# Kernel optimization log

Measured on AMD Instinct MI355X. Metric: run time of the kernel, lower is better.

Reference implementation:

```python
import jax, jax.numpy as jnp
import numpy as np

E = 512; H = 512; L = 3; NH = 8; HD = H // NH; V = 32000
B = 64; S = 64; T = 20


def setup_inputs() -> dict:
    key = jax.random.key(0)
    ks = jax.random.split(key, 14)
    sc = 0.02
    return {
        "encoder_out": jax.random.normal(ks[0], (B, S, H), jnp.float32),
        "captions": jax.random.randint(ks[1], (B, T), 0, V),
        "embed_table": jax.random.normal(ks[2], (V, E), jnp.float32) * sc,
        "w_ih": jax.random.normal(ks[3], (L, 3 * H, E), jnp.float32) * sc,
        "w_hh": jax.random.normal(ks[4], (L, 3 * H, H), jnp.float32) * sc,
        "b_ih": jax.random.normal(ks[5], (L, 3 * H), jnp.float32) * sc,
        "b_hh": jax.random.normal(ks[6], (L, 3 * H), jnp.float32) * sc,
        "in_proj_w": jax.random.normal(ks[7], (3 * H, H), jnp.float32) * sc,
        "in_proj_b": jax.random.normal(ks[8], (3 * H,), jnp.float32) * sc,
        "out_proj_w": jax.random.normal(ks[9], (H, H), jnp.float32) * sc,
        "out_proj_b": jax.random.normal(ks[10], (H,), jnp.float32) * sc,
        "fc_w": jax.random.normal(ks[11], (V, H), jnp.float32) * sc,
        "fc_b": jax.random.normal(ks[12], (V,), jnp.float32) * sc,
    }


def _gru_cell(x, h, Wih, Whh, bih, bhh):
    # PyTorch GRUCell math. x: (B, in), h: (B, H)
    gi = x @ Wih.T + bih  # (B, 3H)
    gh = h @ Whh.T + bhh
    i_r, i_z, i_n = jnp.split(gi, 3, axis=-1)
    h_r, h_z, h_n = jnp.split(gh, 3, axis=-1)
    r = jax.nn.sigmoid(i_r + h_r)
    z = jax.nn.sigmoid(i_z + h_z)
    n = jnp.tanh(i_n + r * h_n)
    return (1.0 - z) * n + z * h


def reference(encoder_out, captions, embed_table, w_ih, w_hh, b_ih, b_hh,
              in_proj_w, in_proj_b, out_proj_w, out_proj_b, fc_w, fc_b):
    Wq, Wk, Wv = jnp.split(in_proj_w, 3, axis=0)
    bq, bk, bv = jnp.split(in_proj_b, 3, axis=0)
    # K/V projections of encoder_out are timestep-invariant: precompute once.
    Kh = (encoder_out @ Wk.T + bk).reshape(B, S, NH, HD)
    Vh = (encoder_out @ Wv.T + bv).reshape(B, S, NH, HD)
    scale = 1.0 / jnp.sqrt(jnp.float32(HD))

    emb = embed_table[captions]              # (B, T, E)
    xs = jnp.transpose(emb, (1, 0, 2))       # (T, B, E)

    def step(h, x_t):
        # h: (L, B, H); x_t: (B, E)
        new_h = []
        inp = x_t
        for l in range(L):
            hl = _gru_cell(inp, h[l], w_ih[l], w_hh[l], b_ih[l], b_hh[l])
            new_h.append(hl)
            inp = hl
        q = (inp @ Wq.T + bq).reshape(B, NH, HD)
        scores = jnp.einsum('bnd,bsnd->bns', q, Kh) * scale
        attn = jax.nn.softmax(scores, axis=-1)
        ctx = jnp.einsum('bns,bsnd->bnd', attn, Vh).reshape(B, H)
        ao = ctx @ out_proj_w.T + out_proj_b
        logits = ao @ fc_w.T + fc_b           # (B, V)
        return jnp.stack(new_h), logits

    h0 = jnp.zeros((L, B, H), dtype=encoder_out.dtype)
    _, logits = jax.lax.scan(step, h0, xs)    # logits: (T, B, V)
    return jnp.transpose(logits, (1, 0, 2))   # (B, T, V)
```

## Files before the change

kernel.cpp:

```cpp
#include <hip/hip_runtime.h>
#include <hip/hip_bf16.h>

#define TT 20
#define BB 64
#define SS 64
#define HH 512
#define EE 512
#define VV 32000

typedef __bf16 bf16x8 __attribute__((ext_vector_type(8)));
typedef float f32x4 __attribute__((ext_vector_type(4)));


__global__ __launch_bounds__(256) void f2bf_kernel(const float* __restrict__ in,
                                                   __hip_bfloat16* __restrict__ out, int n) {
    int i = blockIdx.x * 256 + threadIdx.x;
    if (i < n) out[i] = __float2bfloat16(in[i]);
}

__global__ __launch_bounds__(256) void zero_h_kernel(float* __restrict__ hf,
                                                     __hip_bfloat16* __restrict__ hb, int n) {
    int i = blockIdx.x * 256 + threadIdx.x;
    if (i < n) { hf[i] = 0.f; hb[i] = __float2bfloat16(0.f); }
}

__global__ __launch_bounds__(256) void gather_emb_kernel(const float* __restrict__ tab,
                                                         const int* __restrict__ cap,
                                                         __hip_bfloat16* __restrict__ out) {
    int i = blockIdx.x * 256 + threadIdx.x;
    int e = i & (EE - 1);
    int tb = i >> 9;
    int t = tb >> 6;
    int b = tb & 63;
    int tok = cap[b * TT + t];
    out[i] = __float2bfloat16(tab[(size_t)tok * EE + e]);
}


__global__ __launch_bounds__(256) void gemm_bt_kernel(
    const __hip_bfloat16* __restrict__ A,
    const __hip_bfloat16* __restrict__ Bm,
    const float* __restrict__ bias,
    float* __restrict__ Cf,
    __hip_bfloat16* __restrict__ Cb,
    int K, int ldc, int row_stride, int row_off,
    long sAz, long sBz, long sCz)
{
    A  += (size_t)blockIdx.z * sAz;
    Bm += (size_t)blockIdx.z * sBz;
    long cbase = (long)blockIdx.z * sCz;

    int m0 = blockIdx.x * 64, n0 = blockIdx.y * 64;
    int wave = threadIdx.x >> 6, lane = threadIdx.x & 63;
    int wm = wave & 1, wn = wave >> 1;
    int row16 = lane & 15, quad = lane >> 4;

    const __hip_bfloat16* a0p = A  + (size_t)(m0 + wm * 32 + row16) * K + quad * 8;
    const __hip_bfloat16* a1p = a0p + (size_t)16 * K;
    const __hip_bfloat16* b0p = Bm + (size_t)(n0 + wn * 32 + row16) * K + quad * 8;
    const __hip_bfloat16* b1p = b0p + (size_t)16 * K;

    f32x4 acc00 = {0.f, 0.f, 0.f, 0.f};
    f32x4 acc01 = {0.f, 0.f, 0.f, 0.f};
    f32x4 acc10 = {0.f, 0.f, 0.f, 0.f};
    f32x4 acc11 = {0.f, 0.f, 0.f, 0.f};

    for (int k = 0; k < K; k += 32) {
        bf16x8 a0 = *reinterpret_cast<const bf16x8*>(a0p + k);
        bf16x8 a1 = *reinterpret_cast<const bf16x8*>(a1p + k);
        bf16x8 b0 = *reinterpret_cast<const bf16x8*>(b0p + k);
        bf16x8 b1 = *reinterpret_cast<const bf16x8*>(b1p + k);
        acc00 = __builtin_amdgcn_mfma_f32_16x16x32_bf16(a0, b0, acc00, 0, 0, 0);
        acc01 = __builtin_amdgcn_mfma_f32_16x16x32_bf16(a0, b1, acc01, 0, 0, 0);
        acc10 = __builtin_amdgcn_mfma_f32_16x16x32_bf16(a1, b0, acc10, 0, 0, 0);
        acc11 = __builtin_amdgcn_mfma_f32_16x16x32_bf16(a1, b1, acc11, 0, 0, 0);
    }

    f32x4 accs[2][2] = {{acc00, acc01}, {acc10, acc11}};
#pragma unroll
    for (int mt = 0; mt < 2; ++mt) {
#pragma unroll
        for (int nt = 0; nt < 2; ++nt) {
            int col = n0 + wn * 32 + nt * 16 + row16;
            float bv = bias ? bias[col] : 0.f;
#pragma unroll
            for (int r = 0; r < 4; ++r) {
                int row = m0 + wm * 32 + mt * 16 + quad * 4 + r;
                long off = cbase + (long)(row * row_stride + row_off) * ldc + col;
                float v = accs[mt][nt][r] + bv;
                if (Cb) Cb[off] = __float2bfloat16(v);
                else    Cf[off] = v;
            }
        }
    }
}


__device__ inline float sigmf(float x) { return 1.f / (1.f + __expf(-x)); }

__global__ __launch_bounds__(256) void gru_combine_kernel(
    const float* __restrict__ GI, const float* __restrict__ GH,
    const float* __restrict__ bih, const float* __restrict__ bhh,
    float* __restrict__ h, __hip_bfloat16* __restrict__ hb)
{
    int i = blockIdx.x * 256 + threadIdx.x;
    int b = i >> 9, j = i & 511;
    const float* gi = GI + (size_t)b * 1536;
    const float* gh = GH + (size_t)b * 1536;
    float ir = gi[j]        + bih[j];
    float iz = gi[j + 512]  + bih[j + 512];
    float in_ = gi[j + 1024] + bih[j + 1024];
    float hr = gh[j]        + bhh[j];
    float hz = gh[j + 512]  + bhh[j + 512];
    float hn = gh[j + 1024] + bhh[j + 1024];
    float r = sigmf(ir + hr);
    float z = sigmf(iz + hz);
    float n = tanhf(in_ + r * hn);
    float hv = h[i];
    float hnew = (1.f - z) * n + z * hv;
    h[i] = hnew;
    hb[i] = __float2bfloat16(hnew);
}

__global__ __launch_bounds__(64) void attn_kernel(
    const float* __restrict__ q, const float* __restrict__ KV,
    __hip_bfloat16* __restrict__ ctxb)
{
    int b = blockIdx.x >> 3, nh = blockIdx.x & 7;
    int lane = threadIdx.x;

    const float* qrow = q + (size_t)b * HH + nh * 64;
    const float* kr   = KV + (size_t)(b * 64 + lane) * 1024 + nh * 64;
    float sc = 0.f;
#pragma unroll
    for (int d = 0; d < 64; ++d) sc += qrow[d] * kr[d];
    sc *= 0.125f;

    float m = sc;
    for (int off = 32; off; off >>= 1) m = fmaxf(m, __shfl_xor(m, off, 64));
    float e = __expf(sc - m);
    float s = e;
    for (int off = 32; off; off >>= 1) s += __shfl_xor(s, off, 64);
    float p = e / s;

    __shared__ float pl[64];
    pl[lane] = p;
    __syncthreads();

    float acc = 0.f;
    const float* vb = KV + (size_t)(b * 64) * 1024 + 512 + nh * 64 + lane;
#pragma unroll
    for (int si = 0; si < 64; ++si) acc += pl[si] * vb[(size_t)si * 1024];

    ctxb[(size_t)b * HH + nh * 64 + lane] = __float2bfloat16(acc);
}


extern "C" void kernel_launch(void* const* d_in, const int* in_sizes, int n_in,
                              void* d_out, int out_size, void* d_ws, size_t ws_size,
                              hipStream_t stream) {
    const float* enc        = (const float*)d_in[0];
    const int*   cap        = (const int*)d_in[1];
    const float* emb_tab    = (const float*)d_in[2];
    const float* w_ih       = (const float*)d_in[3];
    const float* w_hh       = (const float*)d_in[4];
    const float* b_ih       = (const float*)d_in[5];
    const float* b_hh       = (const float*)d_in[6];
    const float* in_proj_w  = (const float*)d_in[7];
    const float* in_proj_b  = (const float*)d_in[8];
    const float* out_proj_w = (const float*)d_in[9];
    const float* out_proj_b = (const float*)d_in[10];
    const float* fc_w       = (const float*)d_in[11];
    const float* fc_b       = (const float*)d_in[12];
    float* out = (float*)d_out;

    char* p = (char*)d_ws;
    auto alloc = [&](size_t bytes) {
        char* r = p;
        p += (bytes + 255) & ~(size_t)255;
        return r;
    };
    __hip_bfloat16* fcw_bf  = (__hip_bfloat16*)alloc((size_t)VV * HH * 2);
    __hip_bfloat16* enc_bf  = (__hip_bfloat16*)alloc((size_t)BB * SS * HH * 2);
    __hip_bfloat16* inp_bf  = (__hip_bfloat16*)alloc((size_t)1536 * 512 * 2);
    __hip_bfloat16* wih_bf  = (__hip_bfloat16*)alloc((size_t)3 * 1536 * 512 * 2);
    __hip_bfloat16* whh_bf  = (__hip_bfloat16*)alloc((size_t)3 * 1536 * 512 * 2);
    __hip_bfloat16* wo_bf   = (__hip_bfloat16*)alloc((size_t)512 * 512 * 2);
    __hip_bfloat16* xemb_bf = (__hip_bfloat16*)alloc((size_t)TT * BB * EE * 2);
    float* KV    = (float*)alloc((size_t)4096 * 1024 * 4);
    float* GI0   = (float*)alloc((size_t)1280 * 1536 * 4);
    float* GH    = (float*)alloc((size_t)3 * 64 * 1536 * 4);
    float* GIbuf = (float*)alloc((size_t)64 * 1536 * 4);
    float* hf    = (float*)alloc((size_t)3 * 64 * 512 * 4);
    __hip_bfloat16* hb     = (__hip_bfloat16*)alloc((size_t)3 * 64 * 512 * 2);
    float* qbuf  = (float*)alloc((size_t)64 * 512 * 4);
    __hip_bfloat16* ctx_bf = (__hip_bfloat16*)alloc((size_t)64 * 512 * 2);
    __hip_bfloat16* AO     = (__hip_bfloat16*)alloc((size_t)1280 * 512 * 2);

    auto cvt = [&](const float* src, __hip_bfloat16* dst, int n) {
        f2bf_kernel<<<(n + 255) / 256, 256, 0, stream>>>(src, dst, n);
    };
    cvt(fc_w, fcw_bf, VV * HH);
    cvt(enc, enc_bf, BB * SS * HH);
    cvt(in_proj_w, inp_bf, 1536 * 512);
    cvt(w_ih, wih_bf, 3 * 1536 * 512);
    cvt(w_hh, whh_bf, 3 * 1536 * 512);
    cvt(out_proj_w, wo_bf, 512 * 512);
    gather_emb_kernel<<<(TT * BB * EE) / 256, 256, 0, stream>>>(emb_tab, cap, xemb_bf);
    zero_h_kernel<<<(3 * 64 * 512) / 256, 256, 0, stream>>>(hf, hb, 3 * 64 * 512);

    gemm_bt_kernel<<<dim3(64, 16, 1), 256, 0, stream>>>(
        enc_bf, inp_bf + 512 * 512, in_proj_b + 512, KV, nullptr,
        512, 1024, 1, 0, 0, 0, 0);

    gemm_bt_kernel<<<dim3(20, 24, 1), 256, 0, stream>>>(
        xemb_bf, wih_bf, nullptr, GI0, nullptr,
        512, 1536, 1, 0, 0, 0, 0);

    for (int t = 0; t < TT; ++t) {
        gemm_bt_kernel<<<dim3(1, 24, 3), 256, 0, stream>>>(
            hb, whh_bf, nullptr, GH, nullptr,
            512, 1536, 1, 0, (long)64 * 512, (long)1536 * 512, (long)64 * 1536);

        gru_combine_kernel<<<128, 256, 0, stream>>>(
            GI0 + (size_t)t * 64 * 1536, GH, b_ih, b_hh, hf, hb);
        gemm_bt_kernel<<<dim3(1, 24, 1), 256, 0, stream>>>(
            hb, wih_bf + (size_t)1 * 1536 * 512, nullptr, GIbuf, nullptr,
            512, 1536, 1, 0, 0, 0, 0);
        gru_combine_kernel<<<128, 256, 0, stream>>>(
            GIbuf, GH + 64 * 1536, b_ih + 1536, b_hh + 1536, hf + 64 * 512, hb + 64 * 512);
        gemm_bt_kernel<<<dim3(1, 24, 1), 256, 0, stream>>>(
            hb + 64 * 512, wih_bf + (size_t)2 * 1536 * 512, nullptr, GIbuf, nullptr,
            512, 1536, 1, 0, 0, 0, 0);
        gru_combine_kernel<<<128, 256, 0, stream>>>(
            GIbuf, GH + 2 * 64 * 1536, b_ih + 2 * 1536, b_hh + 2 * 1536,
            hf + 2 * 64 * 512, hb + 2 * 64 * 512);

        gemm_bt_kernel<<<dim3(1, 8, 1), 256, 0, stream>>>(
            hb + 2 * 64 * 512, inp_bf, in_proj_b, qbuf, nullptr,
            512, 512, 1, 0, 0, 0, 0);

        attn_kernel<<<512, 64, 0, stream>>>(qbuf, KV, ctx_bf);

        gemm_bt_kernel<<<dim3(1, 8, 1), 256, 0, stream>>>(
            ctx_bf, wo_bf, out_proj_b, nullptr, AO,
            512, 512, TT, t, 0, 0, 0);
    }

    gemm_bt_kernel<<<dim3(20, 500, 1), 256, 0, stream>>>(
        AO, fcw_bf, fc_b, out, nullptr,
        512, VV, 1, 0, 0, 0, 0);
}
```

Before: 1.860 ms.

## Fuse GRU layers and attention per step, add LDS-staged 128-tile GEMM

Replaces the per-step chain of separate GEMMs and elementwise kernels with one fused kernel per GRU layer (hidden and input projections plus gate math) and one fused attention kernel (query projection, softmax, context, output projection). Hidden state is double-buffered so a layer can read the previous step's bf16 state while writing the next. The large GEMMs move to a new 128x128 tile kernel that stages operands in LDS through global_load_lds. This cuts kernel launches and intermediate global round trips. The cost is very low parallelism: the GRU kernel runs on only 8 blocks, and the attention kernel runs on 64 blocks that each read the full weight matrices with scalar loads.

After: 3.284 ms. +76.6%, slower.

```diff
diff --git a/kernel.cpp b/kernel.cpp
--- a/kernel.cpp
+++ b/kernel.cpp
@@ -11,6 +11,13 @@
 typedef __bf16 bf16x8 __attribute__((ext_vector_type(8)));
 typedef float f32x4 __attribute__((ext_vector_type(4)));
 
+__device__ __forceinline__ void gload_lds16(const __hip_bfloat16* g, __hip_bfloat16* l) {
+    __builtin_amdgcn_global_load_lds((const __attribute__((address_space(1))) void*)g,
+                                     (__attribute__((address_space(3))) void*)l, 16, 0, 0);
+}
+
+__device__ __forceinline__ float sigmf(float x) { return 1.f / (1.f + __expf(-x)); }
+
 
 __global__ __launch_bounds__(256) void f2bf_kernel(const float* __restrict__ in,
                                                    __hip_bfloat16* __restrict__ out, int n) {
@@ -18,10 +25,18 @@
     if (i < n) out[i] = __float2bfloat16(in[i]);
 }
 
+__global__ __launch_bounds__(256) void transpose512_kernel(const float* __restrict__ in,
+                                                           __hip_bfloat16* __restrict__ out) {
+    int i = blockIdx.x * 256 + threadIdx.x;
+    int j = i >> 9, k = i & 511;
+    out[(size_t)k * 512 + j] = __float2bfloat16(in[i]);
+}
+
 __global__ __launch_bounds__(256) void zero_h_kernel(float* __restrict__ hf,
-                                                     __hip_bfloat16* __restrict__ hb, int n) {
+                                                     __hip_bfloat16* __restrict__ hb) {
     int i = blockIdx.x * 256 + threadIdx.x;
-    if (i < n) { hf[i] = 0.f; hb[i] = __float2bfloat16(0.f); }
+    hb[i] = __float2bfloat16(0.f);
+    if (i < 3 * 64 * 512) hf[i] = 0.f;
 }
 
 __global__ __launch_bounds__(256) void gather_emb_kernel(const float* __restrict__ tab,
@@ -37,122 +52,204 @@
 }
 
 
-__global__ __launch_bounds__(256) void gemm_bt_kernel(
+__global__ __launch_bounds__(256) void gemm128_kernel(
     const __hip_bfloat16* __restrict__ A,
     const __hip_bfloat16* __restrict__ Bm,
     const float* __restrict__ bias,
-    float* __restrict__ Cf,
-    __hip_bfloat16* __restrict__ Cb,
-    int K, int ldc, int row_stride, int row_off,
-    long sAz, long sBz, long sCz)
+    float* __restrict__ C,
+    int K, int N)
 {
-    A  += (size_t)blockIdx.z * sAz;
-    Bm += (size_t)blockIdx.z * sBz;
-    long cbase = (long)blockIdx.z * sCz;
-
-    int m0 = blockIdx.x * 64, n0 = blockIdx.y * 64;
+    __shared__ __align__(16) __hip_bfloat16 As[128 * 32];
+    __shared__ __align__(16) __hip_bfloat16 Bs[128 * 32];
+
+    int m0 = blockIdx.x * 128, n0 = blockIdx.y * 128;
+    int tid = threadIdx.x;
+    int wave = tid >> 6, lane = tid & 63;
+    int wm = wave & 1, wn = wave >> 1;
+    int row16 = lane & 15, quad = lane >> 4;
+
+    int r0 = tid >> 2, cc = (tid & 3) * 8;
+    int r1 = 64 + r0;
+    const __hip_bfloat16* gA0 = A  + (size_t)(m0 + r0) * K + cc;
+    const __hip_bfloat16* gA1 = A  + (size_t)(m0 + r1) * K + cc;
+    const __hip_bfloat16* gB0 = Bm + (size_t)(n0 + r0) * K + cc;
+    const __hip_bfloat16* gB1 = Bm + (size_t)(n0 + r1) * K + cc;
+    __hip_bfloat16* lA0 = As + (size_t)(wave * 64) * 8;
+    __hip_bfloat16* lA1 = As + (size_t)(256 + wave * 64) * 8;
+    __hip_bfloat16* lB0 = Bs + (size_t)(wave * 64) * 8;
+    __hip_bfloat16* lB1 = Bs + (size_t)(256 + wave * 64) * 8;
+
+    const __hip_bfloat16* ra = As + (size_t)(wm * 64 + row16) * 32 + quad * 8;
+    const __hip_bfloat16* rb = Bs + (size_t)(wn * 64 + row16) * 32 + quad * 8;
+
+    f32x4 acc[4][4] = {};
+
+    for (int k = 0; k < K; k += 32) {
+        gload_lds16(gA0 + k, lA0);
+        gload_lds16(gA1 + k, lA1);
+        gload_lds16(gB0 + k, lB0);
+        gload_lds16(gB1 + k, lB1);
+        __syncthreads();
+        bf16x8 af[4], bfr[4];
+#pragma unroll
+        for (int mt = 0; mt < 4; ++mt)
+            af[mt] = *reinterpret_cast<const bf16x8*>(ra + mt * 16 * 32);
+#pragma unroll
+        for (int nt = 0; nt < 4; ++nt)
+            bfr[nt] = *reinterpret_cast<const bf16x8*>(rb + nt * 16 * 32);
+#pragma unroll
+        for (int mt = 0; mt < 4; ++mt)
+#pragma unroll
+            for (int nt = 0; nt < 4; ++nt)
+                acc[mt][nt] = __builtin_amdgcn_mfma_f32_16x16x32_bf16(af[mt], bfr[nt], acc[mt][nt], 0, 0, 0);
+        __syncthreads();
+    }
+
+#pragma unroll
+    for (int mt = 0; mt < 4; ++mt)
+#pragma unroll
+        for (int nt = 0; nt < 4; ++nt) {
+            int col = n0 + wn * 64 + nt * 16 + row16;
+            float bv = bias ? bias[col] : 0.f;
+#pragma unroll
+            for (int r = 0; r < 4; ++r) {
+                int row = m0 + wm * 64 + mt * 16 + quad * 4 + r;
+                C[(size_t)row * N + col] = acc[mt][nt][r] + bv;
+            }
+        }
+}
+
+
+__global__ __launch_bounds__(256) void gru_fused_kernel(
+    const __hip_bfloat16* __restrict__ x_bf,
+    const float* __restrict__ GI_pre,
+    const __hip_bfloat16* __restrict__ h_bf,
+    const float* h_f,
+    const __hip_bfloat16* __restrict__ Wih,
+    const __hip_bfloat16* __restrict__ Whh,
+    const float* __restrict__ bih, const float* __restrict__ bhh,
+    float* hf_out, __hip_bfloat16* __restrict__ hb_out)
+{
+    int j0 = blockIdx.x * 64;
     int wave = threadIdx.x >> 6, lane = threadIdx.x & 63;
     int wm = wave & 1, wn = wave >> 1;
     int row16 = lane & 15, quad = lane >> 4;
 
-    const __hip_bfloat16* a0p = A  + (size_t)(m0 + wm * 32 + row16) * K + quad * 8;
-    const __hip_bfloat16* a1p = a0p + (size_t)16 * K;
-    const __hip_bfloat16* b0p = Bm + (size_t)(n0 + wn * 32 + row16) * K + quad * 8;
-    const __hip_bfloat16* b1p = b0p + (size_t)16 * K;
-
-    f32x4 acc00 = {0.f, 0.f, 0.f, 0.f};
-    f32x4 acc01 = {0.f, 0.f, 0.f, 0.f};
-    f32x4 acc10 = {0.f, 0.f, 0.f, 0.f};
-    f32x4 acc11 = {0.f, 0.f, 0.f, 0.f};
-
-    for (int k = 0; k < K; k += 32) {
-        bf16x8 a0 = *reinterpret_cast<const bf16x8*>(a0p + k);
-        bf16x8 a1 = *reinterpret_cast<const bf16x8*>(a1p + k);
-        bf16x8 b0 = *reinterpret_cast<const bf16x8*>(b0p + k);
-        bf16x8 b1 = *reinterpret_cast<const bf16x8*>(b1p + k);
-        acc00 = __builtin_amdgcn_mfma_f32_16x16x32_bf16(a0, b0, acc00, 0, 0, 0);
-        acc01 = __builtin_amdgcn_mfma_f32_16x16x32_bf16(a0, b1, acc01, 0, 0, 0);
-        acc10 = __builtin_amdgcn_mfma_f32_16x16x32_bf16(a1, b0, acc10, 0, 0, 0);
-        acc11 = __builtin_amdgcn_mfma_f32_16x16x32_bf16(a1, b1, acc11, 0, 0, 0);
+    size_t aoff = (size_t)(wm * 32 + row16) * 512 + quad * 8;
+    int bcol = j0 + wn * 32 + row16;
+    size_t boff = (size_t)bcol * 512 + quad * 8;
+
+    f32x4 aR[2][2] = {}, aZ[2][2] = {}, aIN[2][2] = {}, aHN[2][2] = {};
+
+    auto tile = [&](const __hip_bfloat16* Ab, const __hip_bfloat16* Wb, f32x4 (&acc)[2][2]) {
+        const __hip_bfloat16* a0 = Ab + aoff;
+        const __hip_bfloat16* a1 = a0 + 16 * 512;
+        const __hip_bfloat16* b0 = Wb + boff;
+        const __hip_bfloat16* b1 = b0 + 16 * 512;
+#pragma unroll
+        for (int k = 0; k < 512; k += 32) {
+            bf16x8 av0 = *reinterpret_cast<const bf16x8*>(a0 + k);
+            bf16x8 av1 = *reinterpret_cast<const bf16x8*>(a1 + k);
+            bf16x8 bv0 = *reinterpret_cast<const bf16x8*>(b0 + k);
+            bf16x8 bv1 = *reinterpret_cast<const bf16x8*>(b1 + k);
+            acc[0][0] = __builtin_amdgcn_mfma_f32_16x16x32_bf16(av0, bv0, acc[0][0], 0, 0, 0);
+            acc[0][1] = __builtin_amdgcn_mfma_f32_16x16x32_bf16(av0, bv1, acc[0][1], 0, 0, 0);
+            acc[1][0] = __builtin_amdgcn_mfma_f32_16x16x32_bf16(av1, bv0, acc[1][0], 0, 0, 0);
+            acc[1][1] = __builtin_amdgcn_mfma_f32_16x16x32_bf16(av1, bv1, acc[1][1], 0, 0, 0);
+        }
+    };
+
+    tile(h_bf, Whh, aR);
+    tile(h_bf, Whh + (size_t)512 * 512, aZ);
+    tile(h_bf, Whh + (size_t)1024 * 512, aHN);
+    if (!GI_pre) {
+        tile(x_bf, Wih, aR);
+        tile(x_bf, Wih + (size_t)512 * 512, aZ);
+        tile(x_bf, Wih + (size_t)1024 * 512, aIN);
     }
 
-    f32x4 accs[2][2] = {{acc00, acc01}, {acc10, acc11}};
-#pragma unroll
-    for (int mt = 0; mt < 2; ++mt) {
+#pragma unroll
+    for (int mt = 0; mt < 2; ++mt)
 #pragma unroll
         for (int nt = 0; nt < 2; ++nt) {
-            int col = n0 + wn * 32 + nt * 16 + row16;
-            float bv = bias ? bias[col] : 0.f;
+            int col = j0 + wn * 32 + nt * 16 + row16;
+            float b_r  = bih[col] + bhh[col];
+            float b_z  = bih[512 + col] + bhh[512 + col];
+            float bi_n = bih[1024 + col];
+            float bh_n = bhh[1024 + col];
 #pragma unroll
             for (int r = 0; r < 4; ++r) {
-                int row = m0 + wm * 32 + mt * 16 + quad * 4 + r;
-                long off = cbase + (long)(row * row_stride + row_off) * ldc + col;
-                float v = accs[mt][nt][r] + bv;
-                if (Cb) Cb[off] = __float2bfloat16(v);
-                else    Cf[off] = v;
+                int row = wm * 32 + mt * 16 + quad * 4 + r;
+                float vr = aR[mt][nt][r], vz = aZ[mt][nt][r];
+                float vin = aIN[mt][nt][r], vhn = aHN[mt][nt][r];
+                if (GI_pre) {
+                    const float* gp = GI_pre + (size_t)row * 1536 + col;
+                    vr += gp[0]; vz += gp[512]; vin += gp[1024];
+                }
+                float rr = sigmf(vr + b_r);
+                float zz = sigmf(vz + b_z);
+                float nn = tanhf(vin + bi_n + rr * (vhn + bh_n));
+                size_t o = (size_t)row * 512 + col;
+                float hnew = (1.f - zz) * nn + zz * h_f[o];
+                hf_out[o] = hnew;
+                hb_out[o] = __float2bfloat16(hnew);
             }
         }
-    }
-}
-
-
-__device__ inline float sigmf(float x) { return 1.f / (1.f + __expf(-x)); }
-
-__global__ __launch_bounds__(256) void gru_combine_kernel(
-    const float* __restrict__ GI, const float* __restrict__ GH,
-    const float* __restrict__ bih, const float* __restrict__ bhh,
-    float* __restrict__ h, __hip_bfloat16* __restrict__ hb)
+}
+
+
+__global__ __launch_bounds__(512) void attn_fused_kernel(
+    const float* __restrict__ h2,
+    const float* __restrict__ KV,
+    const __hip_bfloat16* __restrict__ WqT,
+    const float* __restrict__ bq,
+    const __hip_bfloat16* __restrict__ WoT,
+    const float* __restrict__ bo,
+    __hip_bfloat16* __restrict__ AO,
+    int t)
 {
-    int i = blockIdx.x * 256 + threadIdx.x;
-    int b = i >> 9, j = i & 511;
-    const float* gi = GI + (size_t)b * 1536;
-    const float* gh = GH + (size_t)b * 1536;
-    float ir = gi[j]        + bih[j];
-    float iz = gi[j + 512]  + bih[j + 512];
-    float in_ = gi[j + 1024] + bih[j + 1024];
-    float hr = gh[j]        + bhh[j];
-    float hz = gh[j + 512]  + bhh[j + 512];
-    float hn = gh[j + 1024] + bhh[j + 1024];
-    float r = sigmf(ir + hr);
-    float z = sigmf(iz + hz);
-    float n = tanhf(in_ + r * hn);
-    float hv = h[i];
-    float hnew = (1.f - z) * n + z * hv;
-    h[i] = hnew;
-    hb[i] = __float2bfloat16(hnew);
-}
-
-__global__ __launch_bounds__(64) void attn_kernel(
-    const float* __restrict__ q, const float* __restrict__ KV,
-    __hip_bfloat16* __restrict__ ctxb)
-{
-    int b = blockIdx.x >> 3, nh = blockIdx.x & 7;
-    int lane = threadIdx.x;
-
-    const float* qrow = q + (size_t)b * HH + nh * 64;
-    const float* kr   = KV + (size_t)(b * 64 + lane) * 1024 + nh * 64;
+    int b = blockIdx.x;
+    int tid = threadIdx.x;
+    __shared__ float qs[512];
+    __shared__ float pl[512];
+    __shared__ float cs[512];
+
+    const float* hrow = h2 + (size_t)b * 512;
+    float qacc = bq[tid];
+#pragma unroll 8
+    for (int k = 0; k < 512; ++k)
+        qacc += hrow[k] * __bfloat162float(WqT[(size_t)k * 512 + tid]);
+    qs[tid] = qacc;
+    __syncthreads();
+
+    int nh = tid >> 6, lane = tid & 63;
+    const float* qh = qs + nh * 64;
+    const float* kr = KV + (size_t)(b * 64 + lane) * 1024 + nh * 64;
     float sc = 0.f;
 #pragma unroll
-    for (int d = 0; d < 64; ++d) sc += qrow[d] * kr[d];
+    for (int d = 0; d < 64; ++d) sc += qh[d] * kr[d];
     sc *= 0.125f;
-
     float m = sc;
     for (int off = 32; off; off >>= 1) m = fmaxf(m, __shfl_xor(m, off, 64));
     float e = __expf(sc - m);
     float s = e;
     for (int off = 32; off; off >>= 1) s += __shfl_xor(s, off, 64);
-    float p = e / s;
-
-    __shared__ float pl[64];
-    pl[lane] = p;
+    pl[tid] = e / s;
     __syncthreads();
 
-    float acc = 0.f;
+    float cacc = 0.f;
+    const float* ph = pl + nh * 64;
     const float* vb = KV + (size_t)(b * 64) * 1024 + 512 + nh * 64 + lane;
 #pragma unroll
-    for (int si = 0; si < 64; ++si) acc += pl[si] * vb[(size_t)si * 1024];
-
-    ctxb[(size_t)b * HH + nh * 64 + lane] = __float2bfloat16(acc);
+    for (int si = 0; si < 64; ++si) cacc += ph[si] * vb[(size_t)si * 1024];
+    cs[tid] = cacc;
+    __syncthreads();
+
+    float ao = bo[tid];
+#pragma unroll 8
+    for (int k = 0; k < 512; ++k)
+        ao += cs[k] * __bfloat162float(WoT[(size_t)k * 512 + tid]);
+    AO[((size_t)b * TT + t) * 512 + tid] = __float2bfloat16(ao);
 }
 
 
@@ -185,17 +282,14 @@
     __hip_bfloat16* inp_bf  = (__hip_bfloat16*)alloc((size_t)1536 * 512 * 2);
     __hip_bfloat16* wih_bf  = (__hip_bfloat16*)alloc((size_t)3 * 1536 * 512 * 2);
     __hip_bfloat16* whh_bf  = (__hip_bfloat16*)alloc((size_t)3 * 1536 * 512 * 2);
-    __hip_bfloat16* wo_bf   = (__hip_bfloat16*)alloc((size_t)512 * 512 * 2);
     __hip_bfloat16* xemb_bf = (__hip_bfloat16*)alloc((size_t)TT * BB * EE * 2);
-    float* KV    = (float*)alloc((size_t)4096 * 1024 * 4);
-    float* GI0   = (float*)alloc((size_t)1280 * 1536 * 4);
-    float* GH    = (float*)alloc((size_t)3 * 64 * 1536 * 4);
-    float* GIbuf = (float*)alloc((size_t)64 * 1536 * 4);
-    float* hf    = (float*)alloc((size_t)3 * 64 * 512 * 4);
-    __hip_bfloat16* hb     = (__hip_bfloat16*)alloc((size_t)3 * 64 * 512 * 2);
-    float* qbuf  = (float*)alloc((size_t)64 * 512 * 4);
-    __hip_bfloat16* ctx_bf = (__hip_bfloat16*)alloc((size_t)64 * 512 * 2);
-    __hip_bfloat16* AO     = (__hip_bfloat16*)alloc((size_t)1280 * 512 * 2);
+    float* KV   = (float*)alloc((size_t)4096 * 1024 * 4);
+    float* GI0  = (float*)alloc((size_t)1280 * 1536 * 4);
+    __hip_bfloat16* WqT = (__hip_bfloat16*)alloc((size_t)512 * 512 * 2);
+    __hip_bfloat16* WoT = (__hip_bfloat16*)alloc((size_t)512 * 512 * 2);
+    float* hf = (float*)alloc((size_t)3 * 64 * 512 * 4);
+    __hip_bfloat16* hb = (__hip_bfloat16*)alloc((size_t)2 * 3 * 64 * 512 * 2);
+    __hip_bfloat16* AO = (__hip_bfloat16*)alloc((size_t)1280 * 512 * 2);
 
     auto cvt = [&](const float* src, __hip_bfloat16* dst, int n) {
         f2bf_kernel<<<(n + 255) / 256, 256, 0, stream>>>(src, dst, n);
@@ -205,49 +299,37 @@
     cvt(in_proj_w, inp_bf, 1536 * 512);
     cvt(w_ih, wih_bf, 3 * 1536 * 512);
     cvt(w_hh, whh_bf, 3 * 1536 * 512);
-    cvt(out_proj_w, wo_bf, 512 * 512);
+    transpose512_kernel<<<1024, 256, 0, stream>>>(in_proj_w, WqT);
+    transpose512_kernel<<<1024, 256, 0, stream>>>(out_proj_w, WoT);
     gather_emb_kernel<<<(TT * BB * EE) / 256, 256, 0, stream>>>(emb_tab, cap, xemb_bf);
-    zero_h_kernel<<<(3 * 64 * 512) / 256, 256, 0, stream>>>(hf, hb, 3 * 64 * 512);
-
-    gemm_bt_kernel<<<dim3(64, 16, 1), 256, 0, stream>>>(
-        enc_bf, inp_bf + 512 * 512, in_proj_b + 512, KV, nullptr,
-        512, 1024, 1, 0, 0, 0, 0);
-
-    gemm_bt_kernel<<<dim3(20, 24, 1), 256, 0, stream>>>(
-        xemb_bf, wih_bf, nullptr, GI0, nullptr,
-        512, 1536, 1, 0, 0, 0, 0);
+    zero_h_kernel<<<(2 * 3 * 64 * 512) / 256, 256, 0, stream>>>(hf, hb);
+
+    gemm128_kernel<<<dim3(32, 8), 256, 0, stream>>>(
+        enc_bf, inp_bf + 512 * 512, in_proj_b + 512, KV, 512, 1024);
+
+    gemm128_kernel<<<dim3(10, 12), 256, 0, stream>>>(
+        xemb_bf, wih_bf, nullptr, GI0, 512, 1536);
+
+    const size_t HS = (size_t)64 * 512;
+    auto hbp = [&](int buf, int l) { return hb + ((size_t)buf * 3 + l) * HS; };
 
     for (int t = 0; t < TT; ++t) {
-        gemm_bt_kernel<<<dim3(1, 24, 3), 256, 0, stream>>>(
-            hb, whh_bf, nullptr, GH, nullptr,
-            512, 1536, 1, 0, (long)64 * 512, (long)1536 * 512, (long)64 * 1536);
-
-        gru_combine_kernel<<<128, 256, 0, stream>>>(
-            GI0 + (size_t)t * 64 * 1536, GH, b_ih, b_hh, hf, hb);
-        gemm_bt_kernel<<<dim3(1, 24, 1), 256, 0, stream>>>(
-            hb, wih_bf + (size_t)1 * 1536 * 512, nullptr, GIbuf, nullptr,
-            512, 1536, 1, 0, 0, 0, 0);
-        gru_combine_kernel<<<128, 256, 0, stream>>>(
-            GIbuf, GH + 64 * 1536, b_ih + 1536, b_hh + 1536, hf + 64 * 512, hb + 64 * 512);
-        gemm_bt_kernel<<<dim3(1, 24, 1), 256, 0, stream>>>(
-            hb + 64 * 512, wih_bf + (size_t)2 * 1536 * 512, nullptr, GIbuf, nullptr,
-            512, 1536, 1, 0, 0, 0, 0);
-        gru_combine_kernel<<<128, 256, 0, stream>>>(
-            GIbuf, GH + 2 * 64 * 1536, b_ih + 2 * 1536, b_hh + 2 * 1536,
-            hf + 2 * 64 * 512, hb + 2 * 64 * 512);
-
-        gemm_bt_kernel<<<dim3(1, 8, 1), 256, 0, stream>>>(
-            hb + 2 * 64 * 512, inp_bf, in_proj_b, qbuf, nullptr,
-            512, 512, 1, 0, 0, 0, 0);
-
-        attn_kernel<<<512, 64, 0, stream>>>(qbuf, KV, ctx_bf);
-
-        gemm_bt_kernel<<<dim3(1, 8, 1), 256, 0, stream>>>(
-            ctx_bf, wo_bf, out_proj_b, nullptr, AO,
-            512, 512, TT, t, 0, 0, 0);
+        int cur = t & 1, nxt = cur ^ 1;
+        gru_fused_kernel<<<8, 256, 0, stream>>>(
+            nullptr, GI0 + (size_t)t * 64 * 1536, hbp(cur, 0), hf,
+            nullptr, whh_bf, b_ih, b_hh, hf, hbp(nxt, 0));
+        gru_fused_kernel<<<8, 256, 0, stream>>>(
+            hbp(nxt, 0), nullptr, hbp(cur, 1), hf + HS,
+            wih_bf + (size_t)1536 * 512, whh_bf + (size_t)1536 * 512,
+            b_ih + 1536, b_hh + 1536, hf + HS, hbp(nxt, 1));
+        gru_fused_kernel<<<8, 256, 0, stream>>>(
+            hbp(nxt, 1), nullptr, hbp(cur, 2), hf + 2 * HS,
+            wih_bf + (size_t)2 * 1536 * 512, whh_bf + (size_t)2 * 1536 * 512,
+            b_ih + 2 * 1536, b_hh + 2 * 1536, hf + 2 * HS, hbp(nxt, 2));
+        attn_fused_kernel<<<64, 512, 0, stream>>>(
+            hf + 2 * HS, KV, WqT, in_proj_b, WoT, out_proj_b, AO, t);
     }
 
-    gemm_bt_kernel<<<dim3(20, 500, 1), 256, 0, stream>>>(
-        AO, fcw_bf, fc_b, out, nullptr,
-        512, VV, 1, 0, 0, 0, 0);
-}
+    gemm128_kernel<<<dim3(10, 250), 256, 0, stream>>>(
+        AO, fcw_bf, fc_b, out, 512, VV);
+}
```
